# Optimization experiments

Hardware: AMD Instinct MI355X
Metric: run time of the kernel (lower is better)

The kernel has to match this reference:

```python
import jax, jax.numpy as jnp
import numpy as np

B, N1, N2 = 8, 2048, 2048
K1D, K2D, V1D, V2D, AD = 256, 256, 256, 256, 128


def setup_inputs() -> dict:
    key = jax.random.key(0)
    ks = jax.random.split(key, 8)
    scale1 = 1.0 / np.sqrt(K1D)
    scale2 = 1.0 / np.sqrt(K2D)
    return {
        "k1": jax.random.normal(ks[0], (B, N1, K1D), jnp.float32),
        "k2": jax.random.normal(ks[1], (B, N2, K2D), jnp.float32),
        "v1": jax.random.normal(ks[2], (B, N1, V1D), jnp.float32),
        "v2": jax.random.normal(ks[3], (B, N2, V2D), jnp.float32),
        "W1": jax.random.uniform(ks[4], (K1D, AD), jnp.float32, -scale1, scale1),
        "b1": jax.random.uniform(ks[5], (AD,), jnp.float32, -scale1, scale1),
        "W2": jax.random.uniform(ks[6], (K2D, AD), jnp.float32, -scale2, scale2),
        "b2": jax.random.uniform(ks[7], (AD,), jnp.float32, -scale2, scale2),
    }


def reference(k1, k2, v1, v2, W1, b1, W2, b2):
    k1p = k1 @ W1 + b1                      # [B, N1, A]
    k2p = k2 @ W2 + b2                      # [B, N2, A]
    score = jnp.einsum("bnd,bmd->bnm", k1p, k2p)   # [B, N1, N2]
    w1 = jax.nn.softmax(score, axis=1)      # softmax over N1 == softmax(score^T, -1)^T
    w2 = jax.nn.softmax(score, axis=-1)     # [B, N1, N2]
    o1 = jnp.einsum("bnm,bnd->bmd", w1, v1)  # [B, N2, V1D]
    o2 = jnp.einsum("bnm,bmd->bnd", w2, v2)  # [B, N1, V2D]
    return (o2, o1)
```

## Files before the change

kernel.cpp:

```cpp
#include <hip/hip_runtime.h>
#include <hip/hip_bf16.h>

#define B_  8
#define N_  2048
#define KD_ 256
#define AD_ 128
#define VD_ 256
#define SQL2E 1.2011224087864498f

using s16x8 = __attribute__((ext_vector_type(8))) short;
using f16x8 = __attribute__((ext_vector_type(8))) _Float16;
using h2    = __attribute__((ext_vector_type(2))) __fp16;
using f32x4 = __attribute__((ext_vector_type(4))) float;

__device__ __forceinline__ f32x4 mfma16(s16x8 a, s16x8 b, f32x4 c) {
  return __builtin_amdgcn_mfma_f32_16x16x32_f16(
      __builtin_bit_cast(f16x8, a), __builtin_bit_cast(f16x8, b), c, 0, 0, 0);
}
__device__ __forceinline__ short f2h(float f) {
  _Float16 h = (_Float16)f;
  return *reinterpret_cast<short*>(&h);
}
__device__ __forceinline__ s16x8 cvt8(const float* __restrict__ p) {
  union { s16x8 v; h2 h[4]; } u;
  f32x4 a = *(const f32x4*)p;
  f32x4 bq = *(const f32x4*)(p + 4);
  u.h[0] = __builtin_amdgcn_cvt_pkrtz(a[0], a[1]);
  u.h[1] = __builtin_amdgcn_cvt_pkrtz(a[2], a[3]);
  u.h[2] = __builtin_amdgcn_cvt_pkrtz(bq[0], bq[1]);
  u.h[3] = __builtin_amdgcn_cvt_pkrtz(bq[2], bq[3]);
  return u.v;
}

__global__ __launch_bounds__(256) void prep_k(
    const float* __restrict__ k1, const float* __restrict__ k2,
    const float* __restrict__ v1, const float* __restrict__ v2,
    const float* __restrict__ W1, const float* __restrict__ b1f,
    const float* __restrict__ W2, const float* __restrict__ b2f,
    short* __restrict__ q1p, short* __restrict__ q2p,
    short* __restrict__ vt1, short* __restrict__ vt2) {
  __shared__ __align__(16) short sWT[128 * 264];
  const int t  = threadIdx.x;
  const int id = blockIdx.x;

  if (id < 512) {
    const int kt = id & 31, b = (id >> 5) & 7, z = id >> 8;
    const float* src = z ? v2 : v1;
    short*       dst = z ? vt2 : vt1;
    const size_t base = ((size_t)(b * 32 + kt)) * (256 * 64);
    const int w = t >> 6, vchunk = (t >> 4) & 3, l16 = t & 15;
    #pragma unroll
    for (int i = 0; i < 8; i++) {
      float x[8];
      #pragma unroll
      for (int kk = 0; kk < 8; kk++)
        x[kk] = src[((size_t)(b * N_ + kt * 64 + i * 8 + kk)) * VD_ + t];
      union { s16x8 v; h2 h[4]; } u;
      #pragma unroll
      for (int kk = 0; kk < 4; kk++)
        u.h[kk] = __builtin_amdgcn_cvt_pkrtz(x[2 * kk], x[2 * kk + 1]);
      int f = vchunk * 2 + (i >> 2);
      *(s16x8*)&dst[base + (size_t)((w * 8 + f) * 64 + (i & 3) * 16 + l16) * 8] = u.v;
    }
    return;
  }

  const int pid = id - 512;
  const int z = pid >> 8, mb = pid & 255;
  const float* X    = z ? k2 : k1;
  const float* W    = z ? W2 : W1;
  const float* bias = z ? b2f : b1f;
  short*       Y    = z ? q2p : q1p;
  const int m0   = mb * 64;
  const int lane = t & 63, wave = t >> 6, quad = lane >> 4, l16 = lane & 15;

  #pragma unroll
  for (int j = 0; j < 64; j++) {
    int idx = j * 256 + t;
    int n = idx & 127, kh = idx >> 7;
    h2 p = __builtin_amdgcn_cvt_pkrtz(W[(size_t)(2 * kh) * AD_ + n] * SQL2E,
                                      W[(size_t)(2 * kh + 1) * AD_ + n] * SQL2E);
    *(h2*)&sWT[n * 264 + kh * 2] = p;
  }
  const float* xrow = &X[(size_t)(m0 + wave * 16 + l16) * KD_];
  s16x8 a[8];
  #pragma unroll
  for (int ks = 0; ks < 8; ks++) a[ks] = cvt8(xrow + ks * 32 + quad * 8);
  __syncthreads();

  f32x4 acc[8];
  #pragma unroll
  for (int nt = 0; nt < 8; nt++) acc[nt] = (f32x4){0.f, 0.f, 0.f, 0.f};
  #pragma unroll
  for (int ks = 0; ks < 8; ks++) {
    #pragma unroll
    for (int nt = 0; nt < 8; nt++) {
      s16x8 bf = *(const s16x8*)&sWT[(nt * 16 + l16) * 264 + ks * 32 + quad * 8];
      acc[nt] = mfma16(a[ks], bf, acc[nt]);
    }
  }
  #pragma unroll
  for (int nt = 0; nt < 8; nt++) {
    float bv = bias[nt * 16 + l16] * SQL2E;
    #pragma unroll
    for (int r = 0; r < 4; r++) {
      int row = m0 + wave * 16 + quad * 4 + r;
      Y[(size_t)row * AD_ + nt * 16 + l16] = f2h(acc[nt][r] + bv);
    }
  }
}

__global__ __launch_bounds__(256, 2) void attn_k(
    const short* __restrict__ q1p, const short* __restrict__ q2p,
    const short* __restrict__ vt1, const short* __restrict__ vt2,
    float* __restrict__ out) {
  __shared__ __align__(16) short sK[2][64 * 136];
  __shared__ __align__(16) short sP[2][4][16 * 64];
  __shared__ __align__(16) float sAl[2][68];

  const int t    = threadIdx.x;
  const int lane = t & 63, wave = t >> 6, quad = lane >> 4, l16 = lane & 15;
  const int id   = blockIdx.x;
  const int xcd  = id & 7, seq = id >> 3;
  const int bp   = xcd * 2 + (seq >> 5);
  const int qb   = seq & 31;
  const int b    = bp & 7, pass = bp >> 3;
  const int q0   = qb * 64;
  const short* Q  = pass ? q2p : q1p;
  const short* K  = pass ? q1p : q2p;
  const short* Vt = pass ? vt1 : vt2;
  float* O = out + (size_t)pass * ((size_t)B_ * N_ * VD_);

  const short* kp = K + (size_t)(b * N_) * AD_ + (size_t)(t >> 4) * AD_ + (t & 15) * 8;
  const short* vp = Vt + (size_t)b * 32 * (256 * 64) + wave * 4096 + lane * 8;

  s16x8 qf[4];
  #pragma unroll
  for (int ks = 0; ks < 4; ks++)
    qf[ks] = *(const s16x8*)&Q[((size_t)(b * N_ + q0 + wave * 16 + l16)) * AD_ +
                               ks * 32 + quad * 8];

  float m_i = -1e30f, l_i = 0.f;
  f32x4 acc[16];
  #pragma unroll
  for (int c0 = 0; c0 < 16; c0++) acc[c0] = (f32x4){0.f, 0.f, 0.f, 0.f};

  s16x8 pk[4], pv[8];
  auto loadK = [&]() {
    #pragma unroll
    for (int i = 0; i < 4; i++) pk[i] = *(const s16x8*)(kp + i * 16 * AD_);
    kp += 64 * AD_;
  };
  auto loadV = [&]() {
    #pragma unroll
    for (int f = 0; f < 8; f++) pv[f] = *(const s16x8*)(vp + f * 512);
    vp += 256 * 64;
  };
  auto storeK = [&](int cb) {
    #pragma unroll
    for (int i = 0; i < 4; i++) {
      int chunk = i * 256 + t, row = chunk >> 4, c8 = chunk & 15;
      *(s16x8*)&sK[cb][row * 136 + c8 * 8] = pk[i];
    }
  };
  auto qk = [&](int cb, f32x4* st) {
    #pragma unroll
    for (int nt = 0; nt < 4; nt++) st[nt] = (f32x4){0.f, 0.f, 0.f, 0.f};
    __builtin_amdgcn_s_setprio(1);
    #pragma unroll
    for (int ks = 0; ks < 4; ks++) {
      #pragma unroll
      for (int nt = 0; nt < 4; nt++) {
        s16x8 kf = *(const s16x8*)&sK[cb][(nt * 16 + l16) * 136 + ks * 32 + quad * 8];
        st[nt] = mfma16(kf, qf[ks], st[nt]);
      }
    }
    __builtin_amdgcn_s_setprio(0);
  };
  auto softmax_store = [&](f32x4* st, int cb) {
    float c0 = fmaxf(fmaxf(st[0][0], st[1][0]), fmaxf(st[2][0], st[3][0]));
    float c1 = fmaxf(fmaxf(st[0][1], st[1][1]), fmaxf(st[2][1], st[3][1]));
    float c2 = fmaxf(fmaxf(st[0][2], st[1][2]), fmaxf(st[2][2], st[3][2]));
    float c3 = fmaxf(fmaxf(st[0][3], st[1][3]), fmaxf(st[2][3], st[3][3]));
    float mt = fmaxf(fmaxf(c0, c1), fmaxf(c2, c3));
    mt = fmaxf(mt, __shfl_xor(mt, 16));
    mt = fmaxf(mt, __shfl_xor(mt, 32));
    float alpha = 1.f;
    bool  resc  = !__all(mt - m_i <= 8.f);
    if (resc) {
      float mn = fmaxf(m_i, mt);
      alpha = exp2f(m_i - mn);
      l_i *= alpha;
      m_i  = mn;
    }
    f32x4 psv = (f32x4){0.f, 0.f, 0.f, 0.f};
    #pragma unroll
    for (int nt = 0; nt < 4; nt++) {
      #pragma unroll
      for (int r = 0; r < 4; r++) {
        float p = exp2f(st[nt][r] - m_i);
        st[nt][r] = p;
        psv[r] += p;
      }
    }
    l_i += (psv[0] + psv[1]) + (psv[2] + psv[3]);
    #pragma unroll
    for (int nt = 0; nt < 4; nt++) {
      union { h2 h[2]; uint2 u; } wu;
      wu.h[0] = __builtin_amdgcn_cvt_pkrtz(st[nt][0], st[nt][1]);
      wu.h[1] = __builtin_amdgcn_cvt_pkrtz(st[nt][2], st[nt][3]);
      int cp = (nt * 4 + quad) ^ ((l16 & 7) << 1);
      *(uint2*)&sP[cb][wave][l16 * 64 + cp * 4] = wu.u;
    }
    if (quad == 0) sAl[cb][wave * 16 + l16] = alpha;
    if (lane == 0) sAl[cb][64 + wave] = resc ? 1.f : 0.f;
  };

  loadK(); storeK(0); loadK(); loadV();
  __syncthreads();
  {
    f32x4 st[4];
    qk(0, st);
    softmax_store(st, 0);
  }
  storeK(1);
  loadK();

  for (int i = 0; i < 32; i++) {
    const int c = i & 1;
    __syncthreads();

    f32x4 st[4];
    if (i + 1 < 32) qk(1 - c, st);

    f32x4 fl = *(const f32x4*)&sAl[c][64];
    if (fl[0] + fl[1] + fl[2] + fl[3] != 0.f) {
      #pragma unroll
      for (int m = 0; m < 4; m++) {
        f32x4 aR = *(const f32x4*)&sAl[c][m * 16 + quad * 4];
        #pragma unroll
        for (int v = 0; v < 4; v++) {
          #pragma unroll
          for (int r = 0; r < 4; r++) acc[m * 4 + v][r] *= aR[r];
        }
      }
    }

    __builtin_amdgcn_s_setprio(1);
    #pragma unroll
    for (int m = 0; m < 4; m++) {
      #pragma unroll
      for (int ks2 = 0; ks2 < 2; ks2++) {
        int cp = (ks2 * 8 + quad * 2) ^ ((l16 & 7) << 1);
        s16x8 af = *(const s16x8*)&sP[c][m][l16 * 64 + cp * 4];
        #pragma unroll
        for (int v = 0; v < 4; v++)
          acc[m * 4 + v] = mfma16(af, pv[v * 2 + ks2], acc[m * 4 + v]);
      }
    }
    __builtin_amdgcn_s_setprio(0);

    if (i + 1 < 32) softmax_store(st, 1 - c);

    if (i + 2 < 32) storeK(c);
    if (i + 3 < 32) loadK();
    if (i + 1 < 32) loadV();
  }

  float lf = l_i + __shfl_xor(l_i, 16);
  lf += __shfl_xor(lf, 32);
  if (quad == 0) sAl[0][wave * 16 + l16] = lf;
  __syncthreads();
  #pragma unroll
  for (int m = 0; m < 4; m++) {
    f32x4 lv = *(const f32x4*)&sAl[0][m * 16 + quad * 4];
    #pragma unroll
    for (int r = 0; r < 4; r++) {
      float inv = 1.f / lv[r];
      int row = q0 + m * 16 + quad * 4 + r;
      #pragma unroll
      for (int v = 0; v < 4; v++)
        O[((size_t)(b * N_ + row)) * VD_ + wave * 64 + v * 16 + l16] =
            acc[m * 4 + v][r] * inv;
    }
  }
}

extern "C" void kernel_launch(void* const* d_in, const int* in_sizes, int n_in,
                              void* d_out, int out_size, void* d_ws, size_t ws_size,
                              hipStream_t stream) {
  const float* k1 = (const float*)d_in[0];
  const float* k2 = (const float*)d_in[1];
  const float* v1 = (const float*)d_in[2];
  const float* v2 = (const float*)d_in[3];
  const float* W1 = (const float*)d_in[4];
  const float* b1 = (const float*)d_in[5];
  const float* W2 = (const float*)d_in[6];
  const float* b2 = (const float*)d_in[7];

  short* ws  = (short*)d_ws;
  short* q1p = ws;
  short* q2p = q1p + (size_t)16384 * 128;
  short* vt1 = q2p + (size_t)16384 * 128;
  short* vt2 = vt1 + (size_t)B_ * 32 * 256 * 64;
  float* out = (float*)d_out;

  prep_k<<<dim3(1024), dim3(256), 0, stream>>>(k1, k2, v1, v2, W1, b1, W2, b2,
                                               q1p, q2p, vt1, vt2);
  attn_k<<<dim3(512), dim3(256), 0, stream>>>(q1p, q2p, vt1, vt2, out);
}
```

Before: 185.4 us.

## Replace software-pipelined QK/softmax with sequential per-tile loop

Removes the one-tile-ahead software pipeline where the QK^T and softmax of the next key tile overlapped the PV MFMA of the current tile, and instead computes QK, softmax, then PV for each tile in order, with one barrier per iteration. K prefetch depth drops from three tiles ahead to two. This lowers register pressure (only one score tile is live) and simplifies the schedule, but gives up the intra-wave overlap between the softmax/exp work and the PV matrix multiply.

```diff
diff --git a/kernel.cpp b/kernel.cpp
--- a/kernel.cpp
+++ b/kernel.cpp
@@ -163,7 +163,13 @@
       *(s16x8*)&sK[cb][row * 136 + c8 * 8] = pk[i];
     }
   };
-  auto qk = [&](int cb, f32x4* st) {
+
+  loadK(); storeK(0); loadK(); loadV();
+  __syncthreads();
+
+  int c = 0;
+  for (int kt = 0; kt < 32; kt++) {
+    f32x4 st[4];
     #pragma unroll
     for (int nt = 0; nt < 4; nt++) st[nt] = (f32x4){0.f, 0.f, 0.f, 0.f};
     __builtin_amdgcn_s_setprio(1);
@@ -171,13 +177,12 @@
     for (int ks = 0; ks < 4; ks++) {
       #pragma unroll
       for (int nt = 0; nt < 4; nt++) {
-        s16x8 kf = *(const s16x8*)&sK[cb][(nt * 16 + l16) * 136 + ks * 32 + quad * 8];
+        s16x8 kf = *(const s16x8*)&sK[c][(nt * 16 + l16) * 136 + ks * 32 + quad * 8];
         st[nt] = mfma16(kf, qf[ks], st[nt]);
       }
     }
     __builtin_amdgcn_s_setprio(0);
-  };
-  auto softmax_store = [&](f32x4* st, int cb) {
+
     float c0 = fmaxf(fmaxf(st[0][0], st[1][0]), fmaxf(st[2][0], st[3][0]));
     float c1 = fmaxf(fmaxf(st[0][1], st[1][1]), fmaxf(st[2][1], st[3][1]));
     float c2 = fmaxf(fmaxf(st[0][2], st[1][2]), fmaxf(st[2][2], st[3][2]));
@@ -185,6 +190,7 @@
     float mt = fmaxf(fmaxf(c0, c1), fmaxf(c2, c3));
     mt = fmaxf(mt, __shfl_xor(mt, 16));
     mt = fmaxf(mt, __shfl_xor(mt, 32));
+
     float alpha = 1.f;
     bool  resc  = !__all(mt - m_i <= 8.f);
     if (resc) {
@@ -193,6 +199,7 @@
       l_i *= alpha;
       m_i  = mn;
     }
+
     f32x4 psv = (f32x4){0.f, 0.f, 0.f, 0.f};
     #pragma unroll
     for (int nt = 0; nt < 4; nt++) {
@@ -204,34 +211,23 @@
       }
     }
     l_i += (psv[0] + psv[1]) + (psv[2] + psv[3]);
+
     #pragma unroll
     for (int nt = 0; nt < 4; nt++) {
       union { h2 h[2]; uint2 u; } wu;
       wu.h[0] = __builtin_amdgcn_cvt_pkrtz(st[nt][0], st[nt][1]);
       wu.h[1] = __builtin_amdgcn_cvt_pkrtz(st[nt][2], st[nt][3]);
       int cp = (nt * 4 + quad) ^ ((l16 & 7) << 1);
-      *(uint2*)&sP[cb][wave][l16 * 64 + cp * 4] = wu.u;
-    }
-    if (quad == 0) sAl[cb][wave * 16 + l16] = alpha;
-    if (lane == 0) sAl[cb][64 + wave] = resc ? 1.f : 0.f;
-  };
-
-  loadK(); storeK(0); loadK(); loadV();
-  __syncthreads();
-  {
-    f32x4 st[4];
-    qk(0, st);
-    softmax_store(st, 0);
-  }
-  storeK(1);
-  loadK();
-
-  for (int i = 0; i < 32; i++) {
-    const int c = i & 1;
+      *(uint2*)&sP[c][wave][l16 * 64 + cp * 4] = wu.u;
+    }
+    if (quad == 0) sAl[c][wave * 16 + l16] = alpha;
+    if (lane == 0) sAl[c][64 + wave] = resc ? 1.f : 0.f;
+
+    if (kt + 1 < 32) storeK(1 - c);
+
     __syncthreads();
 
-    f32x4 st[4];
-    if (i + 1 < 32) qk(1 - c, st);
+    if (kt + 2 < 32) loadK();
 
     f32x4 fl = *(const f32x4*)&sAl[c][64];
     if (fl[0] + fl[1] + fl[2] + fl[3] != 0.f) {
@@ -260,11 +256,8 @@
     }
     __builtin_amdgcn_s_setprio(0);
 
-    if (i + 1 < 32) softmax_store(st, 1 - c);
-
-    if (i + 2 < 32) storeK(c);
-    if (i + 3 < 32) loadK();
-    if (i + 1 < 32) loadV();
+    if (kt + 1 < 32) loadV();
+    c ^= 1;
   }
 
   float lf = l_i + __shfl_xor(l_i, 16);
```

New measurement: 185.1 us. No clear change (-0.2%).
